# Performance work log

Hardware: AMD Instinct MI355X
Metric: run time of the kernel (lower is better)

## Reference

```python
import jax, jax.numpy as jnp
import numpy as np

B, S, D, H, E, K = 8, 2048, 512, 2048, 8, 2


def setup_inputs() -> dict:
    key = jax.random.key(0)
    ks = jax.random.split(key, 6)
    x = jax.random.normal(ks[0], (B, S, D), dtype=jnp.float32)
    # HashRouter output: top-k expert assignments per token (int ids in [0, E))
    assign = jax.random.randint(ks[1], (B, S, K), 0, E, dtype=jnp.int64)
    # Stacked per-expert MLP params: Linear(D,H) -> ReLU -> Linear(H,D)
    s1 = 1.0 / np.sqrt(D)
    s2 = 1.0 / np.sqrt(H)
    W1 = jax.random.uniform(ks[2], (E, D, H), jnp.float32, -s1, s1)
    b1 = jax.random.uniform(ks[3], (E, H), jnp.float32, -s1, s1)
    W2 = jax.random.uniform(ks[4], (E, H, D), jnp.float32, -s2, s2)
    b2 = jax.random.uniform(ks[5], (E, D), jnp.float32, -s2, s2)
    return {"x": x, "assign": assign, "W1": W1, "b1": b1, "W2": W2, "b2": b2}


def reference(x, assign, W1, b1, W2, b2):
    b, s, d = x.shape
    e_total = W1.shape[0]
    k = assign.shape[-1]
    xf = x.reshape(b * s, d)                 # [N, D]
    af = assign.reshape(b * s, k)            # [N, K]
    out = jnp.zeros_like(xf)
    # Loop over fixed, small number of experts (structurally distinct params).
    for e in range(e_total):
        mask = (af == e).any(-1)             # token selected by expert e (once, even if both slots)
        h = jax.nn.relu(xf @ W1[e] + b1[e])  # [N, H]
        y = h @ W2[e] + b2[e]                # [N, D]
        out = out + jnp.where(mask[:, None], y, jnp.zeros((), y.dtype))
    return (out / k).reshape(b, s, d)
```

## Files before the change

kernel.cpp:

```cpp
#include <hip/hip_runtime.h>
#include <hip/hip_bf16.h>
#include <stdint.h>

#define E_NUM 8
#define D_DIM 512
#define H_DIM 2048
#define NTOK 16384

typedef __bf16 bf16;
typedef __bf16 bf16x8 __attribute__((ext_vector_type(8)));
typedef float  f32x4  __attribute__((ext_vector_type(4)));

#define BM 256
#define BN 256
#define BK 64

typedef __attribute__((address_space(1))) const void* gas_cp;
typedef __attribute__((address_space(3))) void* las_p;
__device__ __forceinline__ void gl_lds16(const void* g, void* l) {
  __builtin_amdgcn_global_load_lds((gas_cp)g, (las_p)l, 16, 0, 0);
}

static const size_t OFF_FILL = 32;
static const size_t OFF_LIST = 128;
static const size_t OFF_XBF  = 1ull << 20;
static const size_t OFF_W1T  = OFF_XBF + (size_t)NTOK*D_DIM*2;
static const size_t OFF_W2T  = OFF_W1T + (size_t)E_NUM*H_DIM*D_DIM*2;
static const size_t OFF_HBUF = OFF_W2T + (size_t)E_NUM*H_DIM*D_DIM*2;

__device__ __forceinline__ int rowbase_of(const int* cnt, int e) {
  int acc = 0;
  for (int i = 0; i < e; i++) acc += (cnt[i] + BM - 1) & ~(BM - 1);
  return acc;
}

__global__ void fill_kernel(const int* __restrict__ assign, int* __restrict__ fill,
                            int* __restrict__ lists) {
  int n = blockIdx.x * blockDim.x + threadIdx.x;
  int lane = threadIdx.x & 63;
  unsigned long long below = ((unsigned long long)1 << lane) - 1;
  int e0 = assign[2*n], e1 = assign[2*n+1];
  #pragma unroll
  for (int e = 0; e < E_NUM; e++) {
    bool h0 = (e0 == e);
    bool h1 = (e1 == e) && (e1 != e0);
    unsigned long long m0 = __ballot(h0);
    unsigned long long m1 = __ballot(h1);
    int c = __popcll(m0) + __popcll(m1);
    if (c > 0) {
      int leader = __ffsll((long long)(m0 | m1)) - 1;
      int b = 0;
      if (lane == leader) b = atomicAdd(&fill[e], c);
      b = __shfl(b, leader);
      if (h0) lists[e * NTOK + b + __popcll(m0 & below)] = n;
      if (h1) lists[e * NTOK + b + __popcll(m0) + __popcll(m1 & below)] = n;
    }
  }
}

__global__ void cvt_x(const float* __restrict__ x, bf16* __restrict__ xbf) {
  size_t i = ((size_t)blockIdx.x * 256 + threadIdx.x) * 8;
  float4 a = *reinterpret_cast<const float4*>(x + i);
  float4 b = *reinterpret_cast<const float4*>(x + i + 4);
  bf16x8 o;
  o[0] = (bf16)a.x; o[1] = (bf16)a.y; o[2] = (bf16)a.z; o[3] = (bf16)a.w;
  o[4] = (bf16)b.x; o[5] = (bf16)b.y; o[6] = (bf16)b.z; o[7] = (bf16)b.w;
  *reinterpret_cast<bf16x8*>(xbf + i) = o;
}

__global__ void transpose_cvt(const float* __restrict__ in, bf16* __restrict__ out,
                              int R, int C) {
  __shared__ float tile[32][33];
  int e = blockIdx.z;
  int c0 = blockIdx.x * 32, r0 = blockIdx.y * 32;
  const float* src = in + (size_t)e * R * C;
  bf16* dst = out + (size_t)e * R * C;
  int tx = threadIdx.x, ty = threadIdx.y;
  #pragma unroll
  for (int i = 0; i < 32; i += 8)
    tile[ty + i][tx] = src[(size_t)(r0 + ty + i) * C + c0 + tx];
  __syncthreads();
  #pragma unroll
  for (int i = 0; i < 32; i += 8)
    dst[(size_t)(c0 + ty + i) * R + r0 + tx] = (bf16)tile[tx][ty + i];
}

#define NC1 (H_DIM / BN)
__global__ __launch_bounds__(512, 2) void gemm1(
    const bf16* __restrict__ xbf, const bf16* __restrict__ w1t,
    const float* __restrict__ b1, const int* __restrict__ lists,
    const int* __restrict__ cnt, bf16* __restrict__ hbuf) {
  int lin = blockIdx.x;
  int xcd = lin & 7;
  int rem = lin >> 3;
  int nc  = rem & (NC1 - 1);
  int rb  = (rem >> 3) * 8 + xcd;
  int e   = rb >> 6;
  int m0  = (rb & 63) * BM;
  int ce  = cnt[e];
  if (m0 >= ce) return;
  int n0 = nc * BN;
  int rbase = rowbase_of(cnt, e);

  __shared__ bf16 xs[2][BM * BK];
  __shared__ bf16 bs[2][BN * BK];
  __shared__ int tok[BM];

  int tid = threadIdx.x;
  if (tid < BM) {
    int r = m0 + tid;
    tok[tid] = (r < ce) ? lists[e * NTOK + r] : lists[e * NTOK];
  }
  __syncthreads();

  const bf16* w1e = w1t + (size_t)e * H_DIM * D_DIM + (size_t)n0 * D_DIM;
  int wave = tid >> 6, lane = tid & 63;
  int quad = lane >> 4, l16 = lane & 15;
  int lr = lane >> 3;
  int lcs = (((lane & 7) ^ lr)) * 8;
  int wm = (wave >> 2) * 128, wn = (wave & 3) * 64;
  int l7 = l16 & 7;

  const bf16* asrc[4]; const bf16* bsrc[4]; int soff[4];
  #pragma unroll
  for (int i = 0; i < 4; i++) {
    int s = wave * 4 + i;
    asrc[i] = xbf + (size_t)tok[s * 8 + lr] * D_DIM + lcs;
    bsrc[i] = w1e + (size_t)(s * 8 + lr) * D_DIM + lcs;
    soff[i] = s * 512;
  }
  auto stage = [&](int buf, int k0) {
    #pragma unroll
    for (int i = 0; i < 4; i++) gl_lds16(asrc[i] + k0, &xs[buf][soff[i]]);
    #pragma unroll
    for (int i = 0; i < 4; i++) gl_lds16(bsrc[i] + k0, &bs[buf][soff[i]]);
  };

  f32x4 acc[8][4] = {};
  const int nk = D_DIM / BK;
  stage(0, 0);
  stage(1, BK);
  for (int t = 0; t < nk; t++) {
    if (t + 1 < nk) { asm volatile("s_waitcnt vmcnt(8)" ::: "memory"); }
    else            { asm volatile("s_waitcnt vmcnt(0)" ::: "memory"); }
    __builtin_amdgcn_sched_barrier(0);
    __builtin_amdgcn_s_barrier();
    __builtin_amdgcn_sched_barrier(0);
    const bf16* xsc = xs[t & 1];
    const bf16* bsc = bs[t & 1];
    __builtin_amdgcn_s_setprio(1);
    #pragma unroll
    for (int k2 = 0; k2 < 2; k2++) {
      int sw = ((quad + k2 * 4) ^ l7) * 8;
      bf16x8 bfr[4];
      #pragma unroll
      for (int j = 0; j < 4; j++)
        bfr[j] = *reinterpret_cast<const bf16x8*>(&bsc[(wn + j * 16 + l16) * BK + sw]);
      #pragma unroll
      for (int i = 0; i < 8; i++) {
        bf16x8 af = *reinterpret_cast<const bf16x8*>(&xsc[(wm + i * 16 + l16) * BK + sw]);
        #pragma unroll
        for (int j = 0; j < 4; j++)
          acc[i][j] = __builtin_amdgcn_mfma_f32_16x16x32_bf16(af, bfr[j], acc[i][j], 0, 0, 0);
      }
    }
    __builtin_amdgcn_s_setprio(0);
    __builtin_amdgcn_sched_barrier(0);
    __builtin_amdgcn_s_barrier();
    __builtin_amdgcn_sched_barrier(0);
    if (t + 2 < nk) stage(t & 1, (t + 2) * BK);
  }

  bf16* hrow = hbuf + (size_t)(rbase + m0) * H_DIM;
  #pragma unroll
  for (int i = 0; i < 8; i++) {
    int row = wm + i * 16 + quad * 4;
    #pragma unroll
    for (int j = 0; j < 4; j++) {
      int col = n0 + wn + j * 16 + l16;
      float bias = b1[e * H_DIM + col];
      #pragma unroll
      for (int r = 0; r < 4; r++) {
        float v = acc[i][j][r] + bias;
        v = v > 0.f ? v : 0.f;
        hrow[(size_t)(row + r) * H_DIM + col] = (bf16)v;
      }
    }
  }
}

#define NC2 (D_DIM / BN)
__global__ __launch_bounds__(512, 2) void gemm2(
    const bf16* __restrict__ hbuf, const bf16* __restrict__ w2t,
    const float* __restrict__ b2, const int* __restrict__ lists,
    const int* __restrict__ cnt, float* __restrict__ out) {
  int lin = blockIdx.x;
  int xcd = lin & 7;
  int rem = lin >> 3;
  int nc  = rem & (NC2 - 1);
  int rb  = (rem >> 1) * 8 + xcd;
  int e   = rb >> 6;
  int m0  = (rb & 63) * BM;
  int ce  = cnt[e];
  if (m0 >= ce) return;
  int n0 = nc * BN;
  int rbase = rowbase_of(cnt, e);

  __shared__ bf16 hs[2][BM * BK];
  __shared__ bf16 bs[2][BN * BK];
  __shared__ int tok[BM];

  int tid = threadIdx.x;
  if (tid < BM) {
    int r = m0 + tid;
    tok[tid] = (r < ce) ? lists[e * NTOK + r] : -1;
  }
  __syncthreads();

  const bf16* hbase = hbuf + (size_t)(rbase + m0) * H_DIM;
  const bf16* w2e = w2t + (size_t)e * H_DIM * D_DIM + (size_t)n0 * H_DIM;
  int wave = tid >> 6, lane = tid & 63;
  int quad = lane >> 4, l16 = lane & 15;
  int lr = lane >> 3;
  int lcs = (((lane & 7) ^ lr)) * 8;
  int wm = (wave >> 2) * 128, wn = (wave & 3) * 64;
  int l7 = l16 & 7;

  const bf16* asrc[4]; const bf16* bsrc[4]; int soff[4];
  #pragma unroll
  for (int i = 0; i < 4; i++) {
    int s = wave * 4 + i;
    asrc[i] = hbase + (size_t)(s * 8 + lr) * H_DIM + lcs;
    bsrc[i] = w2e + (size_t)(s * 8 + lr) * H_DIM + lcs;
    soff[i] = s * 512;
  }
  auto stage = [&](int buf, int k0) {
    #pragma unroll
    for (int i = 0; i < 4; i++) gl_lds16(asrc[i] + k0, &hs[buf][soff[i]]);
    #pragma unroll
    for (int i = 0; i < 4; i++) gl_lds16(bsrc[i] + k0, &bs[buf][soff[i]]);
  };

  f32x4 acc[8][4] = {};
  const int nk = H_DIM / BK;
  stage(0, 0);
  stage(1, BK);
  for (int t = 0; t < nk; t++) {
    if (t + 1 < nk) { asm volatile("s_waitcnt vmcnt(8)" ::: "memory"); }
    else            { asm volatile("s_waitcnt vmcnt(0)" ::: "memory"); }
    __builtin_amdgcn_sched_barrier(0);
    __builtin_amdgcn_s_barrier();
    __builtin_amdgcn_sched_barrier(0);
    const bf16* hsc = hs[t & 1];
    const bf16* bsc = bs[t & 1];
    __builtin_amdgcn_s_setprio(1);
    #pragma unroll
    for (int k2 = 0; k2 < 2; k2++) {
      int sw = ((quad + k2 * 4) ^ l7) * 8;
      bf16x8 bfr[4];
      #pragma unroll
      for (int j = 0; j < 4; j++)
        bfr[j] = *reinterpret_cast<const bf16x8*>(&bsc[(wn + j * 16 + l16) * BK + sw]);
      #pragma unroll
      for (int i = 0; i < 8; i++) {
        bf16x8 af = *reinterpret_cast<const bf16x8*>(&hsc[(wm + i * 16 + l16) * BK + sw]);
        #pragma unroll
        for (int j = 0; j < 4; j++)
          acc[i][j] = __builtin_amdgcn_mfma_f32_16x16x32_bf16(af, bfr[j], acc[i][j], 0, 0, 0);
      }
    }
    __builtin_amdgcn_s_setprio(0);
    __builtin_amdgcn_sched_barrier(0);
    __builtin_amdgcn_s_barrier();
    __builtin_amdgcn_sched_barrier(0);
    if (t + 2 < nk) stage(t & 1, (t + 2) * BK);
  }

  #pragma unroll
  for (int i = 0; i < 8; i++) {
    int row = wm + i * 16 + quad * 4;
    #pragma unroll
    for (int j = 0; j < 4; j++) {
      int col = n0 + wn + j * 16 + l16;
      float bias = b2[e * D_DIM + col];
      #pragma unroll
      for (int r = 0; r < 4; r++) {
        int t = tok[row + r];
        if (t >= 0) {
          float v = 0.5f * (acc[i][j][r] + bias);
          atomicAdd(&out[(size_t)t * D_DIM + col], v);
        }
      }
    }
  }
}

extern "C" void kernel_launch(void* const* d_in, const int* in_sizes, int n_in,
                              void* d_out, int out_size, void* d_ws, size_t ws_size,
                              hipStream_t stream) {
  const float* x      = (const float*)d_in[0];
  const int*   assign = (const int*)d_in[1];
  const float* W1     = (const float*)d_in[2];
  const float* b1     = (const float*)d_in[3];
  const float* W2     = (const float*)d_in[4];
  const float* b2     = (const float*)d_in[5];
  float* out = (float*)d_out;
  char* ws = (char*)d_ws;

  int* fill    = (int*)(ws + OFF_FILL);
  int* lists   = (int*)(ws + OFF_LIST);
  bf16* xbf    = (bf16*)(ws + OFF_XBF);
  bf16* w1t    = (bf16*)(ws + OFF_W1T);
  bf16* w2t    = (bf16*)(ws + OFF_W2T);
  bf16* hbuf   = (bf16*)(ws + OFF_HBUF);

  hipMemsetAsync(ws, 0, 128, stream);
  hipMemsetAsync(d_out, 0, (size_t)out_size * sizeof(float), stream);

  fill_kernel<<<NTOK / 256, 256, 0, stream>>>(assign, fill, lists);

  cvt_x<<<(NTOK * D_DIM) / (256 * 8), 256, 0, stream>>>(x, xbf);
  transpose_cvt<<<dim3(H_DIM / 32, D_DIM / 32, E_NUM), dim3(32, 8), 0, stream>>>(W1, w1t, D_DIM, H_DIM);
  transpose_cvt<<<dim3(D_DIM / 32, H_DIM / 32, E_NUM), dim3(32, 8), 0, stream>>>(W2, w2t, H_DIM, D_DIM);

  gemm1<<<(E_NUM * NTOK / BM) * NC1, 512, 0, stream>>>(xbf, w1t, b1, lists, fill, hbuf);
  gemm2<<<(E_NUM * NTOK / BM) * NC2, 512, 0, stream>>>(hbuf, w2t, b2, lists, fill, out);

  (void)in_sizes; (void)n_in; (void)ws_size;
}
```

Measured before the change: 381.4 us.

## Halve BK with new LDS swizzle, raise occupancy, split-K gemm2 by two

```diff
diff --git a/kernel.cpp b/kernel.cpp
--- a/kernel.cpp
+++ b/kernel.cpp
@@ -13,7 +13,7 @@
 
 #define BM 256
 #define BN 256
-#define BK 64
+#define BK 32
 
 typedef __attribute__((address_space(1))) const void* gas_cp;
 typedef __attribute__((address_space(3))) void* las_p;
@@ -85,8 +85,9 @@
     dst[(size_t)(c0 + ty + i) * R + r0 + tx] = (bf16)tile[tx][ty + i];
 }
 
+
 #define NC1 (H_DIM / BN)
-__global__ __launch_bounds__(512, 2) void gemm1(
+__global__ __launch_bounds__(512, 4) void gemm1(
     const bf16* __restrict__ xbf, const bf16* __restrict__ w1t,
     const float* __restrict__ b1, const int* __restrict__ lists,
     const int* __restrict__ cnt, bf16* __restrict__ hbuf) {
@@ -116,24 +117,25 @@
   const bf16* w1e = w1t + (size_t)e * H_DIM * D_DIM + (size_t)n0 * D_DIM;
   int wave = tid >> 6, lane = tid & 63;
   int quad = lane >> 4, l16 = lane & 15;
-  int lr = lane >> 3;
-  int lcs = (((lane & 7) ^ lr)) * 8;
+  int lr = lane >> 2;
+  int ls = lane & 3;
+  int srcoff = ((((ls ^ (lr & 3)) - ((lr >> 2) & 3)) & 3)) * 8;
   int wm = (wave >> 2) * 128, wn = (wave & 3) * 64;
-  int l7 = l16 & 7;
-
-  const bf16* asrc[4]; const bf16* bsrc[4]; int soff[4];
-  #pragma unroll
-  for (int i = 0; i < 4; i++) {
-    int s = wave * 4 + i;
-    asrc[i] = xbf + (size_t)tok[s * 8 + lr] * D_DIM + lcs;
-    bsrc[i] = w1e + (size_t)(s * 8 + lr) * D_DIM + lcs;
+  int rslot = (((quad + ((l16 >> 2) & 3)) & 3) ^ (l16 & 3)) * 8;
+
+  const bf16* asrc[2]; const bf16* bsrc[2]; int soff[2];
+  #pragma unroll
+  for (int i = 0; i < 2; i++) {
+    int s = wave * 2 + i;
+    asrc[i] = xbf + (size_t)tok[s * 16 + lr] * D_DIM + srcoff;
+    bsrc[i] = w1e + (size_t)(s * 16 + lr) * D_DIM + srcoff;
     soff[i] = s * 512;
   }
   auto stage = [&](int buf, int k0) {
     #pragma unroll
-    for (int i = 0; i < 4; i++) gl_lds16(asrc[i] + k0, &xs[buf][soff[i]]);
-    #pragma unroll
-    for (int i = 0; i < 4; i++) gl_lds16(bsrc[i] + k0, &bs[buf][soff[i]]);
+    for (int i = 0; i < 2; i++) gl_lds16(asrc[i] + k0, &xs[buf][soff[i]]);
+    #pragma unroll
+    for (int i = 0; i < 2; i++) gl_lds16(bsrc[i] + k0, &bs[buf][soff[i]]);
   };
 
   f32x4 acc[8][4] = {};
@@ -141,7 +143,7 @@
   stage(0, 0);
   stage(1, BK);
   for (int t = 0; t < nk; t++) {
-    if (t + 1 < nk) { asm volatile("s_waitcnt vmcnt(8)" ::: "memory"); }
+    if (t + 1 < nk) { asm volatile("s_waitcnt vmcnt(4)" ::: "memory"); }
     else            { asm volatile("s_waitcnt vmcnt(0)" ::: "memory"); }
     __builtin_amdgcn_sched_barrier(0);
     __builtin_amdgcn_s_barrier();
@@ -149,16 +151,14 @@
     const bf16* xsc = xs[t & 1];
     const bf16* bsc = bs[t & 1];
     __builtin_amdgcn_s_setprio(1);
-    #pragma unroll
-    for (int k2 = 0; k2 < 2; k2++) {
-      int sw = ((quad + k2 * 4) ^ l7) * 8;
+    {
       bf16x8 bfr[4];
       #pragma unroll
       for (int j = 0; j < 4; j++)
-        bfr[j] = *reinterpret_cast<const bf16x8*>(&bsc[(wn + j * 16 + l16) * BK + sw]);
+        bfr[j] = *reinterpret_cast<const bf16x8*>(&bsc[(wn + j * 16 + l16) * BK + rslot]);
       #pragma unroll
       for (int i = 0; i < 8; i++) {
-        bf16x8 af = *reinterpret_cast<const bf16x8*>(&xsc[(wm + i * 16 + l16) * BK + sw]);
+        bf16x8 af = *reinterpret_cast<const bf16x8*>(&xsc[(wm + i * 16 + l16) * BK + rslot]);
         #pragma unroll
         for (int j = 0; j < 4; j++)
           acc[i][j] = __builtin_amdgcn_mfma_f32_16x16x32_bf16(af, bfr[j], acc[i][j], 0, 0, 0);
@@ -190,7 +190,9 @@
 }
 
 #define NC2 (D_DIM / BN)
-__global__ __launch_bounds__(512, 2) void gemm2(
+#define KSPLIT 2
+#define KHALF (H_DIM / KSPLIT)
+__global__ __launch_bounds__(512, 4) void gemm2(
     const bf16* __restrict__ hbuf, const bf16* __restrict__ w2t,
     const float* __restrict__ b2, const int* __restrict__ lists,
     const int* __restrict__ cnt, float* __restrict__ out) {
@@ -198,7 +200,9 @@
   int xcd = lin & 7;
   int rem = lin >> 3;
   int nc  = rem & (NC2 - 1);
-  int rb  = (rem >> 1) * 8 + xcd;
+  int rem2 = rem >> 1;
+  int kh  = rem2 & (KSPLIT - 1);
+  int rb  = (rem2 >> 1) * 8 + xcd;
   int e   = rb >> 6;
   int m0  = (rb & 63) * BM;
   int ce  = cnt[e];
@@ -217,36 +221,37 @@
   }
   __syncthreads();
 
-  const bf16* hbase = hbuf + (size_t)(rbase + m0) * H_DIM;
-  const bf16* w2e = w2t + (size_t)e * H_DIM * D_DIM + (size_t)n0 * H_DIM;
+  const bf16* hbase = hbuf + (size_t)(rbase + m0) * H_DIM + kh * KHALF;
+  const bf16* w2e = w2t + (size_t)e * H_DIM * D_DIM + (size_t)n0 * H_DIM + kh * KHALF;
   int wave = tid >> 6, lane = tid & 63;
   int quad = lane >> 4, l16 = lane & 15;
-  int lr = lane >> 3;
-  int lcs = (((lane & 7) ^ lr)) * 8;
+  int lr = lane >> 2;
+  int ls = lane & 3;
+  int srcoff = ((((ls ^ (lr & 3)) - ((lr >> 2) & 3)) & 3)) * 8;
   int wm = (wave >> 2) * 128, wn = (wave & 3) * 64;
-  int l7 = l16 & 7;
-
-  const bf16* asrc[4]; const bf16* bsrc[4]; int soff[4];
-  #pragma unroll
-  for (int i = 0; i < 4; i++) {
-    int s = wave * 4 + i;
-    asrc[i] = hbase + (size_t)(s * 8 + lr) * H_DIM + lcs;
-    bsrc[i] = w2e + (size_t)(s * 8 + lr) * H_DIM + lcs;
+  int rslot = (((quad + ((l16 >> 2) & 3)) & 3) ^ (l16 & 3)) * 8;
+
+  const bf16* asrc[2]; const bf16* bsrc[2]; int soff[2];
+  #pragma unroll
+  for (int i = 0; i < 2; i++) {
+    int s = wave * 2 + i;
+    asrc[i] = hbase + (size_t)(s * 16 + lr) * H_DIM + srcoff;
+    bsrc[i] = w2e + (size_t)(s * 16 + lr) * H_DIM + srcoff;
     soff[i] = s * 512;
   }
   auto stage = [&](int buf, int k0) {
     #pragma unroll
-    for (int i = 0; i < 4; i++) gl_lds16(asrc[i] + k0, &hs[buf][soff[i]]);
-    #pragma unroll
-    for (int i = 0; i < 4; i++) gl_lds16(bsrc[i] + k0, &bs[buf][soff[i]]);
+    for (int i = 0; i < 2; i++) gl_lds16(asrc[i] + k0, &hs[buf][soff[i]]);
+    #pragma unroll
+    for (int i = 0; i < 2; i++) gl_lds16(bsrc[i] + k0, &bs[buf][soff[i]]);
   };
 
   f32x4 acc[8][4] = {};
-  const int nk = H_DIM / BK;
+  const int nk = KHALF / BK;
   stage(0, 0);
   stage(1, BK);
   for (int t = 0; t < nk; t++) {
-    if (t + 1 < nk) { asm volatile("s_waitcnt vmcnt(8)" ::: "memory"); }
+    if (t + 1 < nk) { asm volatile("s_waitcnt vmcnt(4)" ::: "memory"); }
     else            { asm volatile("s_waitcnt vmcnt(0)" ::: "memory"); }
     __builtin_amdgcn_sched_barrier(0);
     __builtin_amdgcn_s_barrier();
@@ -254,16 +259,14 @@
     const bf16* hsc = hs[t & 1];
     const bf16* bsc = bs[t & 1];
     __builtin_amdgcn_s_setprio(1);
-    #pragma unroll
-    for (int k2 = 0; k2 < 2; k2++) {
-      int sw = ((quad + k2 * 4) ^ l7) * 8;
+    {
       bf16x8 bfr[4];
       #pragma unroll
       for (int j = 0; j < 4; j++)
-        bfr[j] = *reinterpret_cast<const bf16x8*>(&bsc[(wn + j * 16 + l16) * BK + sw]);
+        bfr[j] = *reinterpret_cast<const bf16x8*>(&bsc[(wn + j * 16 + l16) * BK + rslot]);
       #pragma unroll
       for (int i = 0; i < 8; i++) {
-        bf16x8 af = *reinterpret_cast<const bf16x8*>(&hsc[(wm + i * 16 + l16) * BK + sw]);
+        bf16x8 af = *reinterpret_cast<const bf16x8*>(&hsc[(wm + i * 16 + l16) * BK + rslot]);
         #pragma unroll
         for (int j = 0; j < 4; j++)
           acc[i][j] = __builtin_amdgcn_mfma_f32_16x16x32_bf16(af, bfr[j], acc[i][j], 0, 0, 0);
@@ -282,7 +285,7 @@
     #pragma unroll
     for (int j = 0; j < 4; j++) {
       int col = n0 + wn + j * 16 + l16;
-      float bias = b2[e * D_DIM + col];
+      float bias = (kh == 0) ? b2[e * D_DIM + col] : 0.0f;
       #pragma unroll
       for (int r = 0; r < 4; r++) {
         int t = tok[row + r];
@@ -324,7 +327,7 @@
   transpose_cvt<<<dim3(D_DIM / 32, H_DIM / 32, E_NUM), dim3(32, 8), 0, stream>>>(W2, w2t, H_DIM, D_DIM);
 
   gemm1<<<(E_NUM * NTOK / BM) * NC1, 512, 0, stream>>>(xbf, w1t, b1, lists, fill, hbuf);
-  gemm2<<<(E_NUM * NTOK / BM) * NC2, 512, 0, stream>>>(hbuf, w2t, b2, lists, fill, out);
+  gemm2<<<(E_NUM * NTOK / BM) * NC2 * KSPLIT, 512, 0, stream>>>(hbuf, w2t, b2, lists, fill, out);
 
   (void)in_sizes; (void)n_in; (void)ws_size;
 }
```

Result: slower. 1.309 ms (+243.1%).

## Merge prep kernels and stage gemm1 epilogue through LDS for coalesced stores

Applied to the files above, without the earlier changes.

```diff
diff --git a/kernel.cpp b/kernel.cpp
--- a/kernel.cpp
+++ b/kernel.cpp
@@ -34,45 +34,59 @@
   return acc;
 }
 
-__global__ void fill_kernel(const int* __restrict__ assign, int* __restrict__ fill,
+__global__ void prep_kernel(const float* __restrict__ x, bf16* __restrict__ xbf,
+                            const int* __restrict__ assign, int* __restrict__ fill,
                             int* __restrict__ lists) {
-  int n = blockIdx.x * blockDim.x + threadIdx.x;
-  int lane = threadIdx.x & 63;
-  unsigned long long below = ((unsigned long long)1 << lane) - 1;
-  int e0 = assign[2*n], e1 = assign[2*n+1];
-  #pragma unroll
-  for (int e = 0; e < E_NUM; e++) {
-    bool h0 = (e0 == e);
-    bool h1 = (e1 == e) && (e1 != e0);
-    unsigned long long m0 = __ballot(h0);
-    unsigned long long m1 = __ballot(h1);
-    int c = __popcll(m0) + __popcll(m1);
-    if (c > 0) {
-      int leader = __ffsll((long long)(m0 | m1)) - 1;
-      int b = 0;
-      if (lane == leader) b = atomicAdd(&fill[e], c);
-      b = __shfl(b, leader);
-      if (h0) lists[e * NTOK + b + __popcll(m0 & below)] = n;
-      if (h1) lists[e * NTOK + b + __popcll(m0) + __popcll(m1 & below)] = n;
-    }
-  }
-}
-
-__global__ void cvt_x(const float* __restrict__ x, bf16* __restrict__ xbf) {
-  size_t i = ((size_t)blockIdx.x * 256 + threadIdx.x) * 8;
+  int gid = blockIdx.x * 256 + threadIdx.x;
+  size_t i = (size_t)gid * 8;
   float4 a = *reinterpret_cast<const float4*>(x + i);
   float4 b = *reinterpret_cast<const float4*>(x + i + 4);
   bf16x8 o;
   o[0] = (bf16)a.x; o[1] = (bf16)a.y; o[2] = (bf16)a.z; o[3] = (bf16)a.w;
   o[4] = (bf16)b.x; o[5] = (bf16)b.y; o[6] = (bf16)b.z; o[7] = (bf16)b.w;
   *reinterpret_cast<bf16x8*>(xbf + i) = o;
-}
-
-__global__ void transpose_cvt(const float* __restrict__ in, bf16* __restrict__ out,
-                              int R, int C) {
+
+  if (blockIdx.x < NTOK / 256) {
+    int n = gid;
+    int lane = threadIdx.x & 63;
+    unsigned long long below = ((unsigned long long)1 << lane) - 1;
+    int e0 = assign[2*n], e1 = assign[2*n+1];
+    #pragma unroll
+    for (int e = 0; e < E_NUM; e++) {
+      bool h0 = (e0 == e);
+      bool h1 = (e1 == e) && (e1 != e0);
+      unsigned long long m0 = __ballot(h0);
+      unsigned long long m1 = __ballot(h1);
+      int c = __popcll(m0) + __popcll(m1);
+      if (c > 0) {
+        int leader = __ffsll((long long)(m0 | m1)) - 1;
+        int b2 = 0;
+        if (lane == leader) b2 = atomicAdd(&fill[e], c);
+        b2 = __shfl(b2, leader);
+        if (h0) lists[e * NTOK + b2 + __popcll(m0 & below)] = n;
+        if (h1) lists[e * NTOK + b2 + __popcll(m0) + __popcll(m1 & below)] = n;
+      }
+    }
+  }
+}
+
+#define T1_TILES (E_NUM * (H_DIM/32) * (D_DIM/32))
+__global__ void transpose_cvt2(const float* __restrict__ W1, bf16* __restrict__ w1t,
+                               const float* __restrict__ W2, bf16* __restrict__ w2t) {
   __shared__ float tile[32][33];
-  int e = blockIdx.z;
-  int c0 = blockIdx.x * 32, r0 = blockIdx.y * 32;
+  int bid = blockIdx.x;
+  const float* in; bf16* out; int R, C, bx, by, e;
+  if (bid < T1_TILES) {
+    e = bid >> 10; int rem = bid & 1023;
+    bx = rem & 63; by = rem >> 6;
+    in = W1; out = w1t; R = D_DIM; C = H_DIM;
+  } else {
+    int b2 = bid - T1_TILES;
+    e = b2 >> 10; int rem = b2 & 1023;
+    bx = rem & 15; by = rem >> 4;
+    in = W2; out = w2t; R = H_DIM; C = D_DIM;
+  }
+  int c0 = bx * 32, r0 = by * 32;
   const float* src = in + (size_t)e * R * C;
   bf16* dst = out + (size_t)e * R * C;
   int tx = threadIdx.x, ty = threadIdx.y;
@@ -102,8 +116,7 @@
   int n0 = nc * BN;
   int rbase = rowbase_of(cnt, e);
 
-  __shared__ bf16 xs[2][BM * BK];
-  __shared__ bf16 bs[2][BN * BK];
+  __shared__ bf16 smem[2 * BM * BK + 2 * BN * BK];
   __shared__ int tok[BM];
 
   int tid = threadIdx.x;
@@ -130,10 +143,12 @@
     soff[i] = s * 512;
   }
   auto stage = [&](int buf, int k0) {
-    #pragma unroll
-    for (int i = 0; i < 4; i++) gl_lds16(asrc[i] + k0, &xs[buf][soff[i]]);
-    #pragma unroll
-    for (int i = 0; i < 4; i++) gl_lds16(bsrc[i] + k0, &bs[buf][soff[i]]);
+    bf16* xsb = smem + buf * (BM * BK);
+    bf16* bsb = smem + 2 * (BM * BK) + buf * (BN * BK);
+    #pragma unroll
+    for (int i = 0; i < 4; i++) gl_lds16(asrc[i] + k0, xsb + soff[i]);
+    #pragma unroll
+    for (int i = 0; i < 4; i++) gl_lds16(bsrc[i] + k0, bsb + soff[i]);
   };
 
   f32x4 acc[8][4] = {};
@@ -146,8 +161,8 @@
     __builtin_amdgcn_sched_barrier(0);
     __builtin_amdgcn_s_barrier();
     __builtin_amdgcn_sched_barrier(0);
-    const bf16* xsc = xs[t & 1];
-    const bf16* bsc = bs[t & 1];
+    const bf16* xsc = smem + (t & 1) * (BM * BK);
+    const bf16* bsc = smem + 2 * (BM * BK) + (t & 1) * (BN * BK);
     __builtin_amdgcn_s_setprio(1);
     #pragma unroll
     for (int k2 = 0; k2 < 2; k2++) {
@@ -171,20 +186,33 @@
     if (t + 2 < nk) stage(t & 1, (t + 2) * BK);
   }
 
-  bf16* hrow = hbuf + (size_t)(rbase + m0) * H_DIM;
-  #pragma unroll
-  for (int i = 0; i < 8; i++) {
-    int row = wm + i * 16 + quad * 4;
-    #pragma unroll
-    for (int j = 0; j < 4; j++) {
-      int col = n0 + wn + j * 16 + l16;
-      float bias = b1[e * H_DIM + col];
-      #pragma unroll
-      for (int r = 0; r < 4; r++) {
-        float v = acc[i][j][r] + bias;
-        v = v > 0.f ? v : 0.f;
-        hrow[(size_t)(row + r) * H_DIM + col] = (bf16)v;
-      }
+  {
+    bf16* cs = smem;
+    #pragma unroll
+    for (int i = 0; i < 8; i++) {
+      int row = wm + i * 16 + quad * 4;
+      #pragma unroll
+      for (int j = 0; j < 4; j++) {
+        int col = wn + j * 16 + l16;
+        float bias = b1[e * H_DIM + n0 + col];
+        #pragma unroll
+        for (int r = 0; r < 4; r++) {
+          float v = acc[i][j][r] + bias;
+          v = v > 0.f ? v : 0.f;
+          int rw = row + r;
+          cs[rw * 256 + (col ^ ((rw & 7) << 3))] = (bf16)v;
+        }
+      }
+    }
+    __syncthreads();
+    bf16* hb = hbuf + (size_t)(rbase + m0) * H_DIM + n0;
+    int rr = tid >> 5;
+    int sl = tid & 31;
+    #pragma unroll
+    for (int p = 0; p < 16; p++) {
+      int row = p * 16 + rr;
+      *reinterpret_cast<bf16x8*>(hb + (size_t)row * H_DIM + sl * 8) =
+        *reinterpret_cast<const bf16x8*>(&cs[row * 256 + ((sl ^ (row & 7)) * 8)]);
     }
   }
 }
@@ -317,11 +345,8 @@
   hipMemsetAsync(ws, 0, 128, stream);
   hipMemsetAsync(d_out, 0, (size_t)out_size * sizeof(float), stream);
 
-  fill_kernel<<<NTOK / 256, 256, 0, stream>>>(assign, fill, lists);
-
-  cvt_x<<<(NTOK * D_DIM) / (256 * 8), 256, 0, stream>>>(x, xbf);
-  transpose_cvt<<<dim3(H_DIM / 32, D_DIM / 32, E_NUM), dim3(32, 8), 0, stream>>>(W1, w1t, D_DIM, H_DIM);
-  transpose_cvt<<<dim3(D_DIM / 32, H_DIM / 32, E_NUM), dim3(32, 8), 0, stream>>>(W2, w2t, H_DIM, D_DIM);
+  prep_kernel<<<(NTOK * D_DIM) / (256 * 8), 256, 0, stream>>>(x, xbf, assign, fill, lists);
+  transpose_cvt2<<<2 * T1_TILES, dim3(32, 8), 0, stream>>>(W1, w1t, W2, w2t);
 
   gemm1<<<(E_NUM * NTOK / BM) * NC1, 512, 0, stream>>>(xbf, w1t, b1, lists, fill, hbuf);
   gemm2<<<(E_NUM * NTOK / BM) * NC2, 512, 0, stream>>>(hbuf, w2t, b2, lists, fill, out);
```

Result: no change. 376.8 us (-1.2%).
